# Performance work log

Measured on AMD Instinct MI355X. Metric: run time of the kernel, lower is better.

The kernel has to match this reference:

```python
import jax, jax.numpy as jnp
import numpy as np

BETA_MEM = 0.9
BETA_INH = 0.6
THRESHOLD = 1.0  # snn.Leaky default


def setup_inputs() -> dict:
    key = jax.random.key(0)
    k1, = jax.random.split(key, 1)
    T, B = 1024, 16384
    spike_seq = (jax.random.uniform(k1, (T, B, 2)) < 0.05).astype(jnp.float32)
    w_exc = jnp.array([[0.7, 1.0]], dtype=jnp.float32)  # fc_exc.weight, [1, 2]
    w_inh = jnp.array(-1.0, dtype=jnp.float32)          # scalar inhibitory weight
    return {"spike_seq": spike_seq, "w_exc": w_exc, "w_inh": w_inh}


@jax.custom_vjp
def spike_fn(x):
    # Heaviside spike with ATan surrogate gradient (snntorch default, alpha=2)
    return (x > 0).astype(x.dtype)

def _spike_fwd(x):
    return spike_fn(x), x

def _spike_bwd(x, g):
    return (g / (1.0 + (jnp.pi * x) ** 2),)

spike_fn.defvjp(_spike_fwd, _spike_bwd)


def reference(spike_seq, w_exc, w_inh):
    T, B, _ = spike_seq.shape
    mem0 = jnp.zeros((B, 1), dtype=spike_seq.dtype)
    inh0 = jnp.zeros((B, 1), dtype=spike_seq.dtype)

    def step(carry, x_t):
        mem, inh = carry
        cur_exc = x_t @ w_exc.T                      # [B, 1]
        fm1 = x_t[:, 0:1]                            # [B, 1]
        inh = BETA_INH * inh + fm1
        cur = cur_exc + w_inh * inh
        # snn.Leaky: reset (subtract) computed from previous mem, detached
        reset = jax.lax.stop_gradient((mem - THRESHOLD > 0).astype(mem.dtype))
        mem = BETA_MEM * mem + cur - reset * THRESHOLD
        spk = spike_fn(mem - THRESHOLD)
        return (mem, inh), (spk, mem)

    _, (spk_rec, mem_rec) = jax.lax.scan(step, (mem0, inh0), spike_seq)
    return spk_rec, mem_rec  # each [T, B, 1]
```

## Files before the change

kernel.cpp:

```cpp
#include <hip/hip_runtime.h>

#define T_LEN 1024
#define B_N   16384
#define UNROLL 32

__global__ __launch_bounds__(64, 1) void FMFMNeuronInhib_34033320854098_kernel(
    const float* __restrict__ x,
    const float* __restrict__ w_exc,
    const float* __restrict__ w_inh,
    float* __restrict__ out) {
#pragma clang fp contract(off)
  const int b = blockIdx.x * 64 + threadIdx.x;
  const float w0 = w_exc[0];
  const float w1 = w_exc[1];
  const float wi = w_inh[0];

  float* __restrict__ spk_out = out;
  float* __restrict__ mem_out = out + (size_t)T_LEN * B_N;
  const float2* __restrict__ xp = (const float2*)x + b;

  float mem = 0.0f;
  float inh = 0.0f;

  auto step = [&](int t, float2 xv) {
#pragma clang fp contract(off)
    const float x0 = xv.x;
    const float x1 = xv.y;
    const float cur_exc = x0 * w0 + x1 * w1;
    inh = 0.6f * inh + x0;
    const float cur = cur_exc + wi * inh;
    const float reset = (mem - 1.0f > 0.0f) ? 1.0f : 0.0f;
    mem = 0.9f * mem + cur - reset * 1.0f;
    const float spk = (mem - 1.0f > 0.0f) ? 1.0f : 0.0f;
    __builtin_nontemporal_store(spk, &spk_out[(size_t)t * B_N + b]);
    __builtin_nontemporal_store(mem, &mem_out[(size_t)t * B_N + b]);
  };

  float2 bufA[UNROLL];
  float2 bufB[UNROLL];

#pragma unroll
  for (int u = 0; u < UNROLL; ++u) bufA[u] = xp[(size_t)u * B_N];
  __builtin_amdgcn_sched_barrier(0);

  for (int t0 = 0; t0 < T_LEN; t0 += 2 * UNROLL) {
#pragma unroll
    for (int u = 0; u < UNROLL; ++u)
      bufB[u] = xp[(size_t)(t0 + UNROLL + u) * B_N];
    __builtin_amdgcn_sched_barrier(0);

#pragma unroll
    for (int u = 0; u < UNROLL; ++u) step(t0 + u, bufA[u]);
    __builtin_amdgcn_sched_barrier(0);

    if (t0 + 2 * UNROLL < T_LEN) {
#pragma unroll
      for (int u = 0; u < UNROLL; ++u)
        bufA[u] = xp[(size_t)(t0 + 2 * UNROLL + u) * B_N];
    }
    __builtin_amdgcn_sched_barrier(0);

#pragma unroll
    for (int u = 0; u < UNROLL; ++u) step(t0 + UNROLL + u, bufB[u]);
    __builtin_amdgcn_sched_barrier(0);
  }
}

extern "C" void kernel_launch(void* const* d_in, const int* in_sizes, int n_in,
                              void* d_out, int out_size, void* d_ws, size_t ws_size,
                              hipStream_t stream) {
  const float* x     = (const float*)d_in[0];
  const float* w_exc = (const float*)d_in[1];
  const float* w_inh = (const float*)d_in[2];
  float* out = (float*)d_out;

  dim3 grid(B_N / 64);
  dim3 block(64);
  hipLaunchKernelGGL(FMFMNeuronInhib_34033320854098_kernel, grid, block, 0, stream,
                     x, w_exc, w_inh, out);
}
```

Before: 231.0 us.

## Process two neurons per thread with float4 loads and float2 stores

Each thread now handles two adjacent batch neurons. Inputs are read as float4 and spikes and membrane values are written as float2, which widens each memory access. The prefetch unroll depth is halved to keep register use in check, and the grid shrinks to 128 blocks of 64 threads. This drops the nontemporal store hint and halves the number of waves, so there is less parallelism available to hide memory latency.

```diff
diff --git a/kernel.cpp b/kernel.cpp
--- a/kernel.cpp
+++ b/kernel.cpp
@@ -2,7 +2,9 @@
 
 #define T_LEN 1024
 #define B_N   16384
-#define UNROLL 32
+#define NPT   2
+#define GSZ   (B_N / NPT)
+#define UNROLL 16
 
 __global__ __launch_bounds__(64, 1) void FMFMNeuronInhib_34033320854098_kernel(
     const float* __restrict__ x,
@@ -10,43 +12,51 @@
     const float* __restrict__ w_inh,
     float* __restrict__ out) {
 #pragma clang fp contract(off)
-  const int b = blockIdx.x * 64 + threadIdx.x;
+  const int g = blockIdx.x * 64 + threadIdx.x;
   const float w0 = w_exc[0];
   const float w1 = w_exc[1];
   const float wi = w_inh[0];
 
-  float* __restrict__ spk_out = out;
-  float* __restrict__ mem_out = out + (size_t)T_LEN * B_N;
-  const float2* __restrict__ xp = (const float2*)x + b;
+  const float4* __restrict__ xp = (const float4*)x + g;
+  float2* __restrict__ spk2 = (float2*)out + g;
+  float2* __restrict__ mem2 = (float2*)(out + (size_t)T_LEN * B_N) + g;
 
-  float mem = 0.0f;
-  float inh = 0.0f;
+  float mem_a = 0.0f, inh_a = 0.0f;
+  float mem_b = 0.0f, inh_b = 0.0f;
 
-  auto step = [&](int t, float2 xv) {
+  auto neuron = [&](float x0, float x1, float& mem, float& inh) -> float {
 #pragma clang fp contract(off)
-    const float x0 = xv.x;
-    const float x1 = xv.y;
     const float cur_exc = x0 * w0 + x1 * w1;
     inh = 0.6f * inh + x0;
     const float cur = cur_exc + wi * inh;
-    const float reset = (mem - 1.0f > 0.0f) ? 1.0f : 0.0f;
-    mem = 0.9f * mem + cur - reset * 1.0f;
-    const float spk = (mem - 1.0f > 0.0f) ? 1.0f : 0.0f;
-    __builtin_nontemporal_store(spk, &spk_out[(size_t)t * B_N + b]);
-    __builtin_nontemporal_store(mem, &mem_out[(size_t)t * B_N + b]);
+    const float reset = (mem > 1.0f) ? 1.0f : 0.0f;
+    mem = 0.9f * mem + cur - reset;
+    return (mem > 1.0f) ? 1.0f : 0.0f;
   };
 
-  float2 bufA[UNROLL];
-  float2 bufB[UNROLL];
+  auto step = [&](int t, float4 xv) {
+#pragma clang fp contract(off)
+    float2 s, m;
+    s.x = neuron(xv.x, xv.y, mem_a, inh_a);
+    s.y = neuron(xv.z, xv.w, mem_b, inh_b);
+    m.x = mem_a;
+    m.y = mem_b;
+    const size_t row = (size_t)t * (B_N / 2);
+    spk2[row] = s;
+    mem2[row] = m;
+  };
+
+  float4 bufA[UNROLL];
+  float4 bufB[UNROLL];
 
 #pragma unroll
-  for (int u = 0; u < UNROLL; ++u) bufA[u] = xp[(size_t)u * B_N];
+  for (int u = 0; u < UNROLL; ++u) bufA[u] = xp[(size_t)u * (B_N / 2)];
   __builtin_amdgcn_sched_barrier(0);
 
   for (int t0 = 0; t0 < T_LEN; t0 += 2 * UNROLL) {
 #pragma unroll
     for (int u = 0; u < UNROLL; ++u)
-      bufB[u] = xp[(size_t)(t0 + UNROLL + u) * B_N];
+      bufB[u] = xp[(size_t)(t0 + UNROLL + u) * (B_N / 2)];
     __builtin_amdgcn_sched_barrier(0);
 
 #pragma unroll
@@ -56,7 +66,7 @@
     if (t0 + 2 * UNROLL < T_LEN) {
 #pragma unroll
       for (int u = 0; u < UNROLL; ++u)
-        bufA[u] = xp[(size_t)(t0 + 2 * UNROLL + u) * B_N];
+        bufA[u] = xp[(size_t)(t0 + 2 * UNROLL + u) * (B_N / 2)];
     }
     __builtin_amdgcn_sched_barrier(0);
 
@@ -74,7 +84,7 @@
   const float* w_inh = (const float*)d_in[2];
   float* out = (float*)d_out;
 
-  dim3 grid(B_N / 64);
+  dim3 grid(GSZ / 64);
   dim3 block(64);
   hipLaunchKernelGGL(FMFMNeuronInhib_34033320854098_kernel, grid, block, 0, stream,
                      x, w_exc, w_inh, out);
```

Measured after the change: 252.9 us. 9.5% more time.

## Split into compute and store wavefronts with LDS ring buffer

Applied to the files above, without the earlier changes.

Each block now has one compute wavefront that runs the sequential recurrence and writes spk/mem pairs into a 4-slot LDS ring. Three store wavefronts take turns draining finished phases to global memory, kept in step by block barriers. The aim is to take global store issue off the latency-bound recurrence path and overlap it with compute. In exchange it adds a barrier every 16 steps and LDS traffic, drops the nontemporal stores, and quadruples the threads per block, which may change occupancy.

```diff
diff --git a/kernel.cpp b/kernel.cpp
--- a/kernel.cpp
+++ b/kernel.cpp
@@ -2,67 +2,91 @@
 
 #define T_LEN 1024
 #define B_N   16384
-#define UNROLL 32
+#define PH    16
+#define NPH   (T_LEN / PH)
 
-__global__ __launch_bounds__(64, 1) void FMFMNeuronInhib_34033320854098_kernel(
+__shared__ __align__(16) float2 OUT_lds[4][PH][64];
+
+static __device__ __forceinline__ void block_barrier() {
+  asm volatile("" ::: "memory");
+  __builtin_amdgcn_s_barrier();
+  asm volatile("" ::: "memory");
+}
+
+__global__ __launch_bounds__(256, 1) void FMFMNeuronInhib_34033320854098_kernel(
     const float* __restrict__ x,
     const float* __restrict__ w_exc,
     const float* __restrict__ w_inh,
     float* __restrict__ out) {
 #pragma clang fp contract(off)
-  const int b = blockIdx.x * 64 + threadIdx.x;
-  const float w0 = w_exc[0];
-  const float w1 = w_exc[1];
-  const float wi = w_inh[0];
+  const int lane = threadIdx.x & 63;
+  const int wid  = threadIdx.x >> 6;
+  const int nb0  = blockIdx.x * 64;
 
   float* __restrict__ spk_out = out;
   float* __restrict__ mem_out = out + (size_t)T_LEN * B_N;
-  const float2* __restrict__ xp = (const float2*)x + b;
 
-  float mem = 0.0f;
-  float inh = 0.0f;
+  if (wid == 0) {
+    const float w0 = w_exc[0];
+    const float w1 = w_exc[1];
+    const float wi = w_inh[0];
+    const float2* __restrict__ xp = (const float2*)x + nb0 + lane;
+    float mem = 0.0f, inh = 0.0f;
 
-  auto step = [&](int t, float2 xv) {
-#pragma clang fp contract(off)
-    const float x0 = xv.x;
-    const float x1 = xv.y;
-    const float cur_exc = x0 * w0 + x1 * w1;
-    inh = 0.6f * inh + x0;
-    const float cur = cur_exc + wi * inh;
-    const float reset = (mem - 1.0f > 0.0f) ? 1.0f : 0.0f;
-    mem = 0.9f * mem + cur - reset * 1.0f;
-    const float spk = (mem - 1.0f > 0.0f) ? 1.0f : 0.0f;
-    __builtin_nontemporal_store(spk, &spk_out[(size_t)t * B_N + b]);
-    __builtin_nontemporal_store(mem, &mem_out[(size_t)t * B_N + b]);
-  };
-
-  float2 bufA[UNROLL];
-  float2 bufB[UNROLL];
-
+    float2 bufA[PH], bufB[PH];
 #pragma unroll
-  for (int u = 0; u < UNROLL; ++u) bufA[u] = xp[(size_t)u * B_N];
-  __builtin_amdgcn_sched_barrier(0);
-
-  for (int t0 = 0; t0 < T_LEN; t0 += 2 * UNROLL) {
+    for (int u = 0; u < PH; ++u) bufA[u] = xp[(size_t)u * B_N];
 #pragma unroll
-    for (int u = 0; u < UNROLL; ++u)
-      bufB[u] = xp[(size_t)(t0 + UNROLL + u) * B_N];
+    for (int u = 0; u < PH; ++u) bufB[u] = xp[(size_t)(PH + u) * B_N];
     __builtin_amdgcn_sched_barrier(0);
 
+    auto phase = [&](float2 (&buf)[PH], int p) {
+#pragma clang fp contract(off)
 #pragma unroll
-    for (int u = 0; u < UNROLL; ++u) step(t0 + u, bufA[u]);
-    __builtin_amdgcn_sched_barrier(0);
+      for (int u = 0; u < PH; ++u) {
+        const float x0 = buf[u].x;
+        const float x1 = buf[u].y;
+        const float cur_exc = x0 * w0 + x1 * w1;
+        inh = 0.6f * inh + x0;
+        const float cur = cur_exc + wi * inh;
+        const float reset = (mem > 1.0f) ? 1.0f : 0.0f;
+        mem = 0.9f * mem + cur - reset;
+        const float spk = (mem > 1.0f) ? 1.0f : 0.0f;
+        OUT_lds[p & 3][u][lane] = make_float2(spk, mem);
+      }
+      __builtin_amdgcn_sched_barrier(0);
+      if (p + 2 < NPH) {
+#pragma unroll
+        for (int u = 0; u < PH; ++u)
+          buf[u] = xp[(size_t)((p + 2) * PH + u) * B_N];
+      }
+      __builtin_amdgcn_sched_barrier(0);
+      asm volatile("s_waitcnt lgkmcnt(0)" ::: "memory");
+      block_barrier();
+    };
 
-    if (t0 + 2 * UNROLL < T_LEN) {
+    for (int p = 0; p < NPH; p += 2) {
+      phase(bufA, p);
+      phase(bufB, p + 1);
+    }
+  } else {
+    const int sid = wid - 1;
+    auto drain = [&](int p) {
+      const int tb = p * PH;
+      const int slot = p & 3;
 #pragma unroll
-      for (int u = 0; u < UNROLL; ++u)
-        bufA[u] = xp[(size_t)(t0 + 2 * UNROLL + u) * B_N];
+      for (int u = 0; u < PH; ++u) {
+        const float2 v = OUT_lds[slot][u][lane];
+        const size_t idx = (size_t)(tb + u) * B_N + nb0 + lane;
+        spk_out[idx] = v.x;
+        mem_out[idx] = v.y;
+      }
+    };
+    for (int p = 0; p < NPH; ++p) {
+      if (p >= 1 && ((p - 1) % 3) == sid) drain(p - 1);
+      block_barrier();
     }
-    __builtin_amdgcn_sched_barrier(0);
-
-#pragma unroll
-    for (int u = 0; u < UNROLL; ++u) step(t0 + UNROLL + u, bufB[u]);
-    __builtin_amdgcn_sched_barrier(0);
+    if ((NPH - 1) % 3 == sid) drain(NPH - 1);
   }
 }
 
@@ -75,7 +99,7 @@
   float* out = (float*)d_out;
 
   dim3 grid(B_N / 64);
-  dim3 block(64);
+  dim3 block(256);
   hipLaunchKernelGGL(FMFMNeuronInhib_34033320854098_kernel, grid, block, 0, stream,
                      x, w_exc, w_inh, out);
 }
```

After: 246.8 us. +6.8%, slower.
